# Kernel tuning notes

Measured on AMD Instinct MI355X. Metric: run time of the kernel, lower is better.

The kernel has to match this reference:

```python
import jax, jax.numpy as jnp
import numpy as np

B, S, D = 32, 2048, 1024


def setup_inputs() -> dict:
    key = jax.random.key(0)
    k = jax.random.split(key, 7)
    midi_features = jax.random.normal(k[0], (B, S, D), dtype=jnp.float32)
    scale_id = jax.random.randint(k[1], (B,), 0, 3)
    midi_mask = jax.random.randint(k[2], (B, S), 0, 2).astype(jnp.int32)
    # Stacked branch params: index 0=high, 1=mid, 2=low (matches SCALE_TO_ID)
    W = jax.random.normal(k[3], (3, D, D), dtype=jnp.float32) * 0.02  # Linear weight (out,in)
    b = jax.random.normal(k[4], (3, D), dtype=jnp.float32) * 0.02
    scale_embed = jax.random.normal(k[5], (3, D), dtype=jnp.float32) * 0.02
    branch_embed = jax.random.normal(k[6], (3, D), dtype=jnp.float32) * 0.02
    return {"midi_features": midi_features, "scale_id": scale_id, "midi_mask": midi_mask,
            "W": W, "b": b, "scale_embed": scale_embed, "branch_embed": branch_embed}


def reference(midi_features, scale_id, midi_mask, W, b, scale_embed, branch_embed):
    # Per-sample scale routing: gather the branch's Linear weight for each sample
    # (equivalent to the torch fancy-indexing scatter into out[idx]).
    Wb = W[scale_id]               # (B, D, D) torch Linear convention: y = x @ W.T + b
    bb = b[scale_id]               # (B, D)
    out = jax.nn.silu(jnp.einsum('bsd,bed->bse', midi_features, Wb) + bb[:, None, :])
    # Dropout is identity in eval mode.
    out = out + scale_embed[scale_id][:, None, :]       # (B, S, D)

    seq_mask = midi_mask > 0                             # (B, S) bool
    w = seq_mask.astype(out.dtype)[:, :, None]           # (B, S, 1)
    denom = jnp.maximum(w.sum(axis=1), 1e-6)             # (B, 1)
    low_vec = (out * w).sum(axis=1) / denom              # (B, D) masked mean

    high_cond = out + branch_embed[0]                    # (B, S, D)
    mid_cond = out + branch_embed[1]                     # (B, S, D)
    low_cond = low_vec[:, None, :] + branch_embed[2]     # (B, 1, D) weak_low_alignment=True
    return high_cond, mid_cond, low_cond
```

## Files before the change

### kernel.cpp

```cpp
#include <hip/hip_runtime.h>
#include <hip/hip_bf16.h>

#define B_ 32
#define S_ 2048
#define D_ 1024

#define BM 256
#define BN 128
#define BK 32
#define NKT (D_ / BK)

typedef __attribute__((ext_vector_type(8))) short bf16x8;
typedef __attribute__((ext_vector_type(4))) float f32x4;
typedef __attribute__((ext_vector_type(4))) float float4v;

#define AS1 __attribute__((address_space(1)))
#define AS3 __attribute__((address_space(3)))

__device__ __forceinline__ short f2bf(float f) {
    union { float f; unsigned u; } uf;
    uf.f = f;
    unsigned u = uf.u;
    u += 0x7FFFu + ((u >> 16) & 1u);
    return (short)(u >> 16);
}

__global__ __launch_bounds__(256) void cvt_bf16(const float4v* __restrict__ src,
                                                bf16x8* __restrict__ dst, int n8) {
    const int stride = gridDim.x * blockDim.x;
    for (int i = blockIdx.x * blockDim.x + threadIdx.x; i < n8; i += stride) {
        float4v a = src[2 * i], b = src[2 * i + 1];
        bf16x8 v;
#pragma unroll
        for (int j = 0; j < 4; ++j) {
            v[j]     = f2bf(a[j]);
            v[4 + j] = f2bf(b[j]);
        }
        dst[i] = v;
    }
}


#define STAGE(SB, kt) do {                                                     \
    const __hip_bfloat16* _ga0 = aBase + (size_t)srow * D_ + (kt) * BK + scol; \
    __builtin_amdgcn_global_load_lds((const AS1 unsigned int*)_ga0,            \
        (AS3 unsigned int*)((char*)&As[SB][0] + tid * 16), 16, 0, 0);          \
    const __hip_bfloat16* _ga1 = aBase + (size_t)(srow + 128) * D_ + (kt) * BK + scol; \
    __builtin_amdgcn_global_load_lds((const AS1 unsigned int*)_ga1,            \
        (AS3 unsigned int*)((char*)&As[SB][0] + 8192 + tid * 16), 16, 0, 0);   \
    const __hip_bfloat16* _gb = bBase + (size_t)srow * D_ + (kt) * BK + scol;  \
    __builtin_amdgcn_global_load_lds((const AS1 unsigned int*)_gb,             \
        (AS3 unsigned int*)((char*)&Bs[SB][0] + tid * 16), 16, 0, 0);          \
} while (0)

#define COMPUTE(CB) do {                                                       \
    bf16x8 _af[4], _bv[4];                                                     \
    _Pragma("unroll")                                                          \
    for (int _mi = 0; _mi < 4; ++_mi)                                          \
        _af[_mi] = *(const bf16x8*)((const char*)&As[CB][0] + aRd + _mi * 1024); \
    _Pragma("unroll")                                                          \
    for (int _ni = 0; _ni < 4; ++_ni)                                          \
        _bv[_ni] = *(const bf16x8*)((const char*)&Bs[CB][0] + bRd + _ni * 1024); \
    __builtin_amdgcn_s_setprio(1);                                             \
    _Pragma("unroll")                                                          \
    for (int _mi = 0; _mi < 4; ++_mi)                                          \
        _Pragma("unroll")                                                      \
        for (int _ni = 0; _ni < 4; ++_ni)                                      \
            acc[_mi][_ni] = __builtin_amdgcn_mfma_f32_16x16x32_bf16(           \
                _af[_mi], _bv[_ni], acc[_mi][_ni], 0, 0, 0);                   \
    __builtin_amdgcn_s_setprio(0); } while (0)

#define VMW(n)  asm volatile("s_waitcnt vmcnt(" #n ")" ::: "memory")
#define SBAR()  asm volatile("s_barrier" ::: "memory")

#define KITER(CB, SB, ktn) do { VMW(3); SBAR(); STAGE(SB, ktn); COMPUTE(CB); } while (0)

__global__ __launch_bounds__(512, 4) void fused_gemm_bf16(
    const __hip_bfloat16* __restrict__ aBf,
    const __hip_bfloat16* __restrict__ wBf,
    const int*   __restrict__ scale_id,
    const int*   __restrict__ mask,
    const float* __restrict__ bias,
    const float* __restrict__ scemb,
    const float* __restrict__ bremb,
    float*       __restrict__ out,
    float*       __restrict__ colws)
{
    __shared__ __align__(16) short As[3][BM * BK];
    __shared__ __align__(16) short Bs[3][BN * BK];

    const int tid = threadIdx.x;
    const int lane = tid & 63;
    const int wid = tid >> 6;
    const int wm = wid >> 1, wn = wid & 1;

    const int NTI = D_ / BN;
    const int MTI = S_ / BM;
    const int NWG = B_ * MTI * NTI;
    const int CPX = NWG / 8;
    int lid = ((int)blockIdx.x % 8) * CPX + ((int)blockIdx.x / 8);
    int nt = lid % NTI;
    int mt = (lid / NTI) % MTI;
    int bb = lid / (NTI * MTI);

    const int sid = scale_id[bb];
    const __hip_bfloat16* aBase = aBf + ((size_t)bb * S_ + (size_t)mt * BM) * D_;
    const __hip_bfloat16* bBase = wBf + ((size_t)sid * D_ + (size_t)nt * BN) * D_;

    const int l5 = tid & 31;
    const int ir0 = ((l5 >> 2) ^ (l5 >> 4)) & 1;
    const int ir1 = (l5 >> 3) & 1;
    const int ir2 = (l5 >> 4) & 1;
    const int is1 = ((l5 >> 1) ^ (l5 >> 3)) & 1;
    const int is0 = (l5 ^ (l5 >> 2) ^ (l5 >> 4)) & 1;
    const int srow = (tid >> 5) * 8 + ir2 * 4 + ir1 * 2 + ir0;
    const int scol = (is1 * 2 + is0) * 8;

    const int fr = lane & 15;
    const int fg = lane >> 4;
    const int aRd = (((wm * 64 + fr) * 64) + fg * 16) ^ ((fr & 7) << 4);
    const int bRd = (((wn * 64 + fr) * 64) + fg * 16) ^ ((fr & 7) << 4);

    f32x4 acc[4][4];
#pragma unroll
    for (int mi = 0; mi < 4; ++mi)
#pragma unroll
        for (int ni = 0; ni < 4; ++ni)
            acc[mi][ni] = (f32x4){0.f, 0.f, 0.f, 0.f};

    STAGE(0, 0);
    STAGE(1, 1);

#pragma unroll 1
    for (int t = 0; t < NKT - 2; t += 3) {
        KITER(0, 2, t + 2);
        KITER(1, 0, t + 3);
        KITER(2, 1, t + 4);
    }
    VMW(3); SBAR(); COMPUTE(0);
    VMW(0); SBAR(); COMPUTE(1);

    __syncthreads();

    const int colb = nt * BN;
    float bv[4], sv[4];
#pragma unroll
    for (int ni = 0; ni < 4; ++ni) {
        const int n = colb + wn * 64 + ni * 16 + fr;
        bv[ni] = bias[sid * D_ + n];
        sv[ni] = scemb[sid * D_ + n];
    }

    float colsum[4] = {0.f, 0.f, 0.f, 0.f};
#pragma unroll
    for (int mi = 0; mi < 4; ++mi) {
        const int mrow0 = mt * BM + wm * 64 + mi * 16 + fg * 4;
        float mk[4];
#pragma unroll
        for (int r = 0; r < 4; ++r)
            mk[r] = (mask[(size_t)bb * S_ + mrow0 + r] > 0) ? 1.f : 0.f;
#pragma unroll
        for (int ni = 0; ni < 4; ++ni)
#pragma unroll
            for (int r = 0; r < 4; ++r) {
                const float v = acc[mi][ni][r] + bv[ni];
                const float o = v / (1.f + __expf(-v)) + sv[ni];
                acc[mi][ni][r] = o;
                colsum[ni] += mk[r] * o;
            }
    }

#pragma unroll
    for (int ni = 0; ni < 4; ++ni) {
        float s = colsum[ni];
        s += __shfl_xor(s, 16);
        s += __shfl_xor(s, 32);
        if (fg == 0) {
            const int n = colb + wn * 64 + ni * 16 + fr;
            atomicAdd(&colws[(size_t)bb * D_ + n], s);
        }
    }

    float* ldsF = (float*)&As[0][0];
    const int lr = tid >> 3;
    const int c8 = tid & 7;

    float4v b0q[4], b1q[4];
#pragma unroll
    for (int q = 0; q < 4; ++q) {
        const int gcol = colb + q * 32 + c8 * 4;
        b0q[q] = *(const float4v*)&bremb[0 * D_ + gcol];
        b1q[q] = *(const float4v*)&bremb[1 * D_ + gcol];
    }

    const size_t MIDOFF = (size_t)B_ * S_ * D_;

#pragma unroll
    for (int mi = 0; mi < 4; ++mi) {
#pragma unroll
        for (int ni = 0; ni < 4; ++ni)
#pragma unroll
            for (int r = 0; r < 4; ++r)
                ldsF[(wm * 16 + fg * 4 + r) * 132 + wn * 64 + ni * 16 + fr] =
                    acc[mi][ni][r];
        __syncthreads();

        const int grow = mt * BM + (lr >> 4) * 64 + mi * 16 + (lr & 15);
        const size_t rowbase = ((size_t)bb * S_ + grow) * D_ + colb;
#pragma unroll
        for (int q = 0; q < 4; ++q) {
            float4v v = *(const float4v*)&ldsF[lr * 132 + q * 32 + c8 * 4];
            __builtin_nontemporal_store(v + b0q[q], (float4v*)&out[rowbase + q * 32 + c8 * 4]);
            __builtin_nontemporal_store(v + b1q[q], (float4v*)&out[MIDOFF + rowbase + q * 32 + c8 * 4]);
        }
        __syncthreads();
    }
}

#define FBM 128
#define FBN 128
#define FBK 64
#define FNK (D_ / FBK)

__global__ __launch_bounds__(256, 2) void fused_gemm_f32(
    const float* __restrict__ midi,
    const int*   __restrict__ scale_id,
    const int*   __restrict__ mask,
    const float* __restrict__ W,
    const float* __restrict__ bias,
    const float* __restrict__ scemb,
    const float* __restrict__ bremb,
    float*       __restrict__ out,
    float*       __restrict__ ws)
{
    __shared__ __align__(16) short Asf[FBM * FBK];
    __shared__ __align__(16) short Bsf[FBM * FBK];

    const int tid = threadIdx.x;
    const int NTI = D_ / FBN;
    const int MTI = S_ / FBM;
    const int NWG = B_ * MTI * NTI;
    const int CPX = NWG / 8;
    int lid = ((int)blockIdx.x % 8) * CPX + ((int)blockIdx.x / 8);
    int nt = lid % NTI;
    int mt = (lid / NTI) % MTI;
    int bb = lid / (NTI * MTI);

    const int sid = scale_id[bb];
    const float* aBase = midi + ((size_t)bb * S_ + (size_t)mt * FBM) * D_;
    const float* bBase = W + ((size_t)sid * D_ + (size_t)nt * FBN) * D_;

    const int r0 = tid >> 3;
    const int kp = (tid & 7) * 8;

    float4v aL[4], aH[4], bL[4], bH[4];

    auto load_regs = [&](int kt) {
        const int kc = kt * FBK + kp;
#pragma unroll
        for (int i = 0; i < 4; ++i) {
            const float* pa = aBase + (size_t)(r0 + 32 * i) * D_ + kc;
            aL[i] = *(const float4v*)pa;
            aH[i] = *(const float4v*)(pa + 4);
            const float* pb = bBase + (size_t)(r0 + 32 * i) * D_ + kc;
            bL[i] = *(const float4v*)pb;
            bH[i] = *(const float4v*)(pb + 4);
        }
    };

    auto write_lds = [&]() {
#pragma unroll
        for (int i = 0; i < 4; ++i) {
            const int row = r0 + 32 * i;
            const int off = (row * FBK + kp) ^ ((row & 7) << 3);
            bf16x8 va, vb;
#pragma unroll
            for (int j = 0; j < 4; ++j) {
                va[j]     = f2bf(aL[i][j]);
                va[4 + j] = f2bf(aH[i][j]);
                vb[j]     = f2bf(bL[i][j]);
                vb[4 + j] = f2bf(bH[i][j]);
            }
            *(bf16x8*)&Asf[off] = va;
            *(bf16x8*)&Bsf[off] = vb;
        }
    };

    f32x4 acc[4][4];
#pragma unroll
    for (int mi = 0; mi < 4; ++mi)
#pragma unroll
        for (int ni = 0; ni < 4; ++ni)
            acc[mi][ni] = (f32x4){0.f, 0.f, 0.f, 0.f};

    const int lane = tid & 63;
    const int wid = tid >> 6;
    const int wm = wid >> 1, wn = wid & 1;
    const int fr = lane & 15;
    const int fg = lane >> 4;

    load_regs(0);
    write_lds();
    __syncthreads();

    for (int kt = 0; kt < FNK; ++kt) {
        if (kt + 1 < FNK) load_regs(kt + 1);
#pragma unroll
        for (int kk = 0; kk < 2; ++kk) {
            bf16x8 af[4], bfr[4];
#pragma unroll
            for (int mi = 0; mi < 4; ++mi) {
                const int row = wm * 64 + mi * 16 + fr;
                const int off = (row * FBK + kk * 32 + fg * 8) ^ ((row & 7) << 3);
                af[mi] = *(const bf16x8*)&Asf[off];
            }
#pragma unroll
            for (int ni = 0; ni < 4; ++ni) {
                const int row = wn * 64 + ni * 16 + fr;
                const int off = (row * FBK + kk * 32 + fg * 8) ^ ((row & 7) << 3);
                bfr[ni] = *(const bf16x8*)&Bsf[off];
            }
#pragma unroll
            for (int mi = 0; mi < 4; ++mi)
#pragma unroll
                for (int ni = 0; ni < 4; ++ni)
                    acc[mi][ni] = __builtin_amdgcn_mfma_f32_16x16x32_bf16(
                        af[mi], bfr[ni], acc[mi][ni], 0, 0, 0);
        }
        __syncthreads();
        if (kt + 1 < FNK) write_lds();
        __syncthreads();
    }

    const int ncolbase = nt * FBN + wn * 64;
    float bv[4], sv[4], b0v[4], b1v[4];
#pragma unroll
    for (int ni = 0; ni < 4; ++ni) {
        const int n = ncolbase + ni * 16 + fr;
        bv[ni]  = bias[sid * D_ + n];
        sv[ni]  = scemb[sid * D_ + n];
        b0v[ni] = bremb[0 * D_ + n];
        b1v[ni] = bremb[1 * D_ + n];
    }

    const size_t MIDOFF = (size_t)B_ * S_ * D_;
    float colsum[4] = {0.f, 0.f, 0.f, 0.f};

#pragma unroll
    for (int mi = 0; mi < 4; ++mi) {
        const int mrow0 = mt * FBM + wm * 64 + mi * 16 + fg * 4;
        float mk[4];
#pragma unroll
        for (int r = 0; r < 4; ++r)
            mk[r] = (mask[(size_t)bb * S_ + mrow0 + r] > 0) ? 1.f : 0.f;
#pragma unroll
        for (int ni = 0; ni < 4; ++ni) {
            const int n = ncolbase + ni * 16 + fr;
#pragma unroll
            for (int r = 0; r < 4; ++r) {
                const float v = acc[mi][ni][r] + bv[ni];
                const float o = v / (1.f + __expf(-v)) + sv[ni];
                const size_t idx = ((size_t)bb * S_ + (size_t)(mrow0 + r)) * D_ + n;
                __builtin_nontemporal_store(o + b0v[ni], &out[idx]);
                __builtin_nontemporal_store(o + b1v[ni], &out[MIDOFF + idx]);
                colsum[ni] += mk[r] * o;
            }
        }
    }

#pragma unroll
    for (int ni = 0; ni < 4; ++ni) {
        float s = colsum[ni];
        s += __shfl_xor(s, 16);
        s += __shfl_xor(s, 32);
        if (fg == 0)
            atomicAdd(&ws[(size_t)bb * D_ + (ncolbase + ni * 16 + fr)], s);
    }
}

__global__ void finalize(const int* __restrict__ mask,
                         const float* __restrict__ ws,
                         const float* __restrict__ bremb,
                         float* __restrict__ out)
{
    const int b = blockIdx.x;
    const int tid = threadIdx.x;

    int c = 0;
    for (int s = tid; s < S_; s += 256)
        c += (mask[(size_t)b * S_ + s] > 0) ? 1 : 0;
#pragma unroll
    for (int m = 1; m < 64; m <<= 1)
        c += __shfl_xor(c, m);

    __shared__ int part[4];
    if ((tid & 63) == 0) part[tid >> 6] = c;
    __syncthreads();
    const float denom = fmaxf((float)(part[0] + part[1] + part[2] + part[3]), 1e-6f);
    const float inv = 1.f / denom;

    const size_t LOWOFF = (size_t)2 * B_ * S_ * D_;
    for (int e = tid; e < D_; e += 256)
        out[LOWOFF + (size_t)b * D_ + e] = ws[(size_t)b * D_ + e] * inv + bremb[2 * D_ + e];
}

extern "C" void kernel_launch(void* const* d_in, const int* in_sizes, int n_in,
                              void* d_out, int out_size, void* d_ws, size_t ws_size,
                              hipStream_t stream) {
    const float* midi     = (const float*)d_in[0];
    const int*   scale_id = (const int*)d_in[1];
    const int*   mask     = (const int*)d_in[2];
    const float* W        = (const float*)d_in[3];
    const float* bias     = (const float*)d_in[4];
    const float* scemb    = (const float*)d_in[5];
    const float* bremb    = (const float*)d_in[6];
    float* out = (float*)d_out;
    float* colws = (float*)d_ws;

    const size_t COLWS_B = (size_t)B_ * D_ * sizeof(float);
    const size_t WBF_B   = (size_t)3 * D_ * D_ * sizeof(short);
    const size_t ABF_B   = (size_t)B_ * S_ * D_ * sizeof(short);
    const size_t need    = COLWS_B + WBF_B + ABF_B;

    hipMemsetAsync(colws, 0, COLWS_B, stream);

    if (ws_size >= need) {
        __hip_bfloat16* wBf = (__hip_bfloat16*)((char*)d_ws + COLWS_B);
        __hip_bfloat16* aBf = (__hip_bfloat16*)((char*)d_ws + COLWS_B + WBF_B);
        cvt_bf16<<<dim3(2048), dim3(256), 0, stream>>>(
            (const float4v*)midi, (bf16x8*)aBf, (B_ * S_ * D_) / 8);
        cvt_bf16<<<dim3(512), dim3(256), 0, stream>>>(
            (const float4v*)W, (bf16x8*)wBf, (3 * D_ * D_) / 8);
        fused_gemm_bf16<<<dim3(B_ * (S_ / BM) * (D_ / BN)), dim3(512), 0, stream>>>(
            aBf, wBf, scale_id, mask, bias, scemb, bremb, out, colws);
    } else {
        fused_gemm_f32<<<dim3(B_ * (S_ / FBM) * (D_ / FBN)), dim3(256), 0, stream>>>(
            midi, scale_id, mask, W, bias, scemb, bremb, out, colws);
    }

    finalize<<<dim3(B_), dim3(256), 0, stream>>>(mask, colws, bremb, out);
}
```

Measured before the change: 345.5 us.

## Retile bf16 GEMM to 256x64x64 with 4 waves and split-phase double buffering

Changes the bf16 GEMM tile from 256x128 with BK=32 and 8 waves to 256x64 with BK=64 and 4 waves. Each wave now computes two 64-row halves, and the A/B stage loads are split across two half-iterations so loads overlap with compute on a two-buffer LDS ring. The LDS swizzle and the epilogue store layout are redone to match the new tile. Narrower N tiles double the grid size and re-read A twice as often, traded for lower LDS footprint and finer-grained load/compute interleaving.

```diff
diff --git a/kernel.cpp b/kernel.cpp
--- a/kernel.cpp
+++ b/kernel.cpp
@@ -6,8 +6,8 @@
 #define D_ 1024
 
 #define BM 256
-#define BN 128
-#define BK 32
+#define BN 64
+#define BK 64
 #define NKT (D_ / BK)
 
 typedef __attribute__((ext_vector_type(8))) short bf16x8;
@@ -41,41 +41,69 @@
 }
 
 
-#define STAGE(SB, kt) do {                                                     \
-    const __hip_bfloat16* _ga0 = aBase + (size_t)srow * D_ + (kt) * BK + scol; \
-    __builtin_amdgcn_global_load_lds((const AS1 unsigned int*)_ga0,            \
-        (AS3 unsigned int*)((char*)&As[SB][0] + tid * 16), 16, 0, 0);          \
-    const __hip_bfloat16* _ga1 = aBase + (size_t)(srow + 128) * D_ + (kt) * BK + scol; \
-    __builtin_amdgcn_global_load_lds((const AS1 unsigned int*)_ga1,            \
-        (AS3 unsigned int*)((char*)&As[SB][0] + 8192 + tid * 16), 16, 0, 0);   \
-    const __hip_bfloat16* _gb = bBase + (size_t)srow * D_ + (kt) * BK + scol;  \
-    __builtin_amdgcn_global_load_lds((const AS1 unsigned int*)_gb,             \
-        (AS3 unsigned int*)((char*)&Bs[SB][0] + tid * 16), 16, 0, 0);          \
-} while (0)
-
-#define COMPUTE(CB) do {                                                       \
-    bf16x8 _af[4], _bv[4];                                                     \
+#define STAGE_A(nb, p, kt) do {                                                \
     _Pragma("unroll")                                                          \
-    for (int _mi = 0; _mi < 4; ++_mi)                                          \
-        _af[_mi] = *(const bf16x8*)((const char*)&As[CB][0] + aRd + _mi * 1024); \
+    for (int _j = 0; _j < 4; ++_j) {                                           \
+        const int _r = (_j >> 1) * 128 + (p) * 64 + (_j & 1) * 32 + wid * 8 + lrow8; \
+        const __hip_bfloat16* _g = aBase + (size_t)_r * D_ + (kt) * BK + (scb >> 1); \
+        __builtin_amdgcn_global_load_lds((const AS1 unsigned int*)_g,          \
+            (AS3 unsigned int*)&As[nb][_r * 64 + (lane & 7) * 8], 16, 0, 0);   \
+    } } while (0)
+
+#define STAGE_B(nb, kt) do {                                                   \
     _Pragma("unroll")                                                          \
-    for (int _ni = 0; _ni < 4; ++_ni)                                          \
-        _bv[_ni] = *(const bf16x8*)((const char*)&Bs[CB][0] + bRd + _ni * 1024); \
+    for (int _j = 0; _j < 2; ++_j) {                                           \
+        const int _r = _j * 32 + wid * 8 + lrow8;                              \
+        const __hip_bfloat16* _g = bBase + (size_t)_r * D_ + (kt) * BK + (scb >> 1); \
+        __builtin_amdgcn_global_load_lds((const AS1 unsigned int*)_g,          \
+            (AS3 unsigned int*)&Bs[nb][_r * 64 + (lane & 7) * 8], 16, 0, 0);   \
+    } } while (0)
+
+#define COMPUTE(cur, p) do {                                                   \
+    bf16x8 _af[4][2], _bv[2][2];                                               \
+    _Pragma("unroll")                                                          \
+    for (int _mi = 0; _mi < 4; ++_mi) {                                        \
+        const int _l = wm * 128 + (p) * 64 + _mi * 16 + fr;                    \
+        _Pragma("unroll")                                                      \
+        for (int _kk = 0; _kk < 2; ++_kk) {                                    \
+            const int _b = _l * 128 + ((_kk * 64 + fg * 16) ^ ((_l & 7) << 4)); \
+            _af[_mi][_kk] = *(const bf16x8*)((const char*)&As[cur][0] + _b);   \
+        }                                                                      \
+    }                                                                          \
+    _Pragma("unroll")                                                          \
+    for (int _ni = 0; _ni < 2; ++_ni) {                                        \
+        const int _l = wn * 32 + _ni * 16 + fr;                                \
+        _Pragma("unroll")                                                      \
+        for (int _kk = 0; _kk < 2; ++_kk) {                                    \
+            const int _b = _l * 128 + ((_kk * 64 + fg * 16) ^ ((_l & 7) << 4)); \
+            _bv[_ni][_kk] = *(const bf16x8*)((const char*)&Bs[cur][0] + _b);   \
+        }                                                                      \
+    }                                                                          \
     __builtin_amdgcn_s_setprio(1);                                             \
     _Pragma("unroll")                                                          \
     for (int _mi = 0; _mi < 4; ++_mi)                                          \
         _Pragma("unroll")                                                      \
-        for (int _ni = 0; _ni < 4; ++_ni)                                      \
-            acc[_mi][_ni] = __builtin_amdgcn_mfma_f32_16x16x32_bf16(           \
-                _af[_mi], _bv[_ni], acc[_mi][_ni], 0, 0, 0);                   \
+        for (int _ni = 0; _ni < 2; ++_ni)                                      \
+            _Pragma("unroll")                                                  \
+            for (int _kk = 0; _kk < 2; ++_kk)                                  \
+                acc[p][_mi][_ni] = __builtin_amdgcn_mfma_f32_16x16x32_bf16(    \
+                    _af[_mi][_kk], _bv[_ni][_kk], acc[p][_mi][_ni], 0, 0, 0);  \
     __builtin_amdgcn_s_setprio(0); } while (0)
 
 #define VMW(n)  asm volatile("s_waitcnt vmcnt(" #n ")" ::: "memory")
 #define SBAR()  asm volatile("s_barrier" ::: "memory")
 
-#define KITER(CB, SB, ktn) do { VMW(3); SBAR(); STAGE(SB, ktn); COMPUTE(CB); } while (0)
-
-__global__ __launch_bounds__(512, 4) void fused_gemm_bf16(
+#define KITER(X, Y, ktn) do {                                                  \
+    STAGE_A(Y, 0, ktn); VMW(8);  SBAR(); COMPUTE(X, 0);                        \
+    STAGE_B(Y, ktn); STAGE_A(Y, 1, ktn); VMW(10); SBAR(); COMPUTE(X, 1);       \
+} while (0)
+
+#define KTAIL(X) do {                                                          \
+    VMW(4); SBAR(); COMPUTE(X, 0);                                             \
+    VMW(0); SBAR(); COMPUTE(X, 1);                                             \
+} while (0)
+
+__global__ __launch_bounds__(256, 2) void fused_gemm_bf16(
     const __hip_bfloat16* __restrict__ aBf,
     const __hip_bfloat16* __restrict__ wBf,
     const int*   __restrict__ scale_id,
@@ -86,8 +114,8 @@
     float*       __restrict__ out,
     float*       __restrict__ colws)
 {
-    __shared__ __align__(16) short As[3][BM * BK];
-    __shared__ __align__(16) short Bs[3][BN * BK];
+    __shared__ __align__(16) short As[2][BM * BK];
+    __shared__ __align__(16) short Bs[2][BN * BK];
 
     const int tid = threadIdx.x;
     const int lane = tid & 63;
@@ -107,114 +135,105 @@
     const __hip_bfloat16* aBase = aBf + ((size_t)bb * S_ + (size_t)mt * BM) * D_;
     const __hip_bfloat16* bBase = wBf + ((size_t)sid * D_ + (size_t)nt * BN) * D_;
 
-    const int l5 = tid & 31;
-    const int ir0 = ((l5 >> 2) ^ (l5 >> 4)) & 1;
-    const int ir1 = (l5 >> 3) & 1;
-    const int ir2 = (l5 >> 4) & 1;
-    const int is1 = ((l5 >> 1) ^ (l5 >> 3)) & 1;
-    const int is0 = (l5 ^ (l5 >> 2) ^ (l5 >> 4)) & 1;
-    const int srow = (tid >> 5) * 8 + ir2 * 4 + ir1 * 2 + ir0;
-    const int scol = (is1 * 2 + is0) * 8;
+    const int lrow8 = lane >> 3;
+    const int scb = ((lane & 7) * 16) ^ (lrow8 << 4);
 
     const int fr = lane & 15;
     const int fg = lane >> 4;
-    const int aRd = (((wm * 64 + fr) * 64) + fg * 16) ^ ((fr & 7) << 4);
-    const int bRd = (((wn * 64 + fr) * 64) + fg * 16) ^ ((fr & 7) << 4);
-
-    f32x4 acc[4][4];
-#pragma unroll
-    for (int mi = 0; mi < 4; ++mi)
-#pragma unroll
-        for (int ni = 0; ni < 4; ++ni)
-            acc[mi][ni] = (f32x4){0.f, 0.f, 0.f, 0.f};
-
-    STAGE(0, 0);
-    STAGE(1, 1);
+
+    f32x4 acc[2][4][2];
+#pragma unroll
+    for (int p = 0; p < 2; ++p)
+#pragma unroll
+        for (int mi = 0; mi < 4; ++mi)
+#pragma unroll
+            for (int ni = 0; ni < 2; ++ni)
+                acc[p][mi][ni] = (f32x4){0.f, 0.f, 0.f, 0.f};
+
+    STAGE_A(0, 0, 0);
+    STAGE_B(0, 0);
+    STAGE_A(0, 1, 0);
 
 #pragma unroll 1
-    for (int t = 0; t < NKT - 2; t += 3) {
-        KITER(0, 2, t + 2);
-        KITER(1, 0, t + 3);
-        KITER(2, 1, t + 4);
-    }
-    VMW(3); SBAR(); COMPUTE(0);
-    VMW(0); SBAR(); COMPUTE(1);
-
+    for (int t = 0; t < NKT - 2; t += 2) {
+        KITER(0, 1, t + 1);
+        KITER(1, 0, t + 2);
+    }
+    KITER(0, 1, NKT - 1);
+    KTAIL(1);
+
+    asm volatile("s_waitcnt vmcnt(0) lgkmcnt(0)" ::: "memory");
     __syncthreads();
 
     const int colb = nt * BN;
-    float bv[4], sv[4];
-#pragma unroll
-    for (int ni = 0; ni < 4; ++ni) {
-        const int n = colb + wn * 64 + ni * 16 + fr;
+    float bv[2], sv[2];
+#pragma unroll
+    for (int ni = 0; ni < 2; ++ni) {
+        const int n = colb + wn * 32 + ni * 16 + fr;
         bv[ni] = bias[sid * D_ + n];
         sv[ni] = scemb[sid * D_ + n];
     }
 
-    float colsum[4] = {0.f, 0.f, 0.f, 0.f};
-#pragma unroll
-    for (int mi = 0; mi < 4; ++mi) {
-        const int mrow0 = mt * BM + wm * 64 + mi * 16 + fg * 4;
-        float mk[4];
-#pragma unroll
-        for (int r = 0; r < 4; ++r)
-            mk[r] = (mask[(size_t)bb * S_ + mrow0 + r] > 0) ? 1.f : 0.f;
-#pragma unroll
-        for (int ni = 0; ni < 4; ++ni)
-#pragma unroll
-            for (int r = 0; r < 4; ++r) {
-                const float v = acc[mi][ni][r] + bv[ni];
-                const float o = v / (1.f + __expf(-v)) + sv[ni];
-                acc[mi][ni][r] = o;
-                colsum[ni] += mk[r] * o;
-            }
-    }
-
-#pragma unroll
-    for (int ni = 0; ni < 4; ++ni) {
+    float colsum[2] = {0.f, 0.f};
+#pragma unroll
+    for (int p = 0; p < 2; ++p)
+#pragma unroll
+        for (int mi = 0; mi < 4; ++mi) {
+            const int mrow0 = mt * BM + wm * 128 + p * 64 + mi * 16 + fg * 4;
+            float mk[4];
+#pragma unroll
+            for (int r = 0; r < 4; ++r)
+                mk[r] = (mask[(size_t)bb * S_ + mrow0 + r] > 0) ? 1.f : 0.f;
+#pragma unroll
+            for (int ni = 0; ni < 2; ++ni)
+#pragma unroll
+                for (int r = 0; r < 4; ++r) {
+                    const float v = acc[p][mi][ni][r] + bv[ni];
+                    const float o = v / (1.f + __expf(-v)) + sv[ni];
+                    acc[p][mi][ni][r] = o;
+                    colsum[ni] += mk[r] * o;
+                }
+        }
+
+#pragma unroll
+    for (int ni = 0; ni < 2; ++ni) {
         float s = colsum[ni];
         s += __shfl_xor(s, 16);
         s += __shfl_xor(s, 32);
         if (fg == 0) {
-            const int n = colb + wn * 64 + ni * 16 + fr;
+            const int n = colb + wn * 32 + ni * 16 + fr;
             atomicAdd(&colws[(size_t)bb * D_ + n], s);
         }
     }
 
     float* ldsF = (float*)&As[0][0];
-    const int lr = tid >> 3;
-    const int c8 = tid & 7;
-
-    float4v b0q[4], b1q[4];
-#pragma unroll
-    for (int q = 0; q < 4; ++q) {
-        const int gcol = colb + q * 32 + c8 * 4;
-        b0q[q] = *(const float4v*)&bremb[0 * D_ + gcol];
-        b1q[q] = *(const float4v*)&bremb[1 * D_ + gcol];
-    }
-
+    const float4v b0 = *(const float4v*)&bremb[0 * D_ + colb + (tid & 15) * 4];
+    const float4v b1 = *(const float4v*)&bremb[1 * D_ + colb + (tid & 15) * 4];
     const size_t MIDOFF = (size_t)B_ * S_ * D_;
 
 #pragma unroll
-    for (int mi = 0; mi < 4; ++mi) {
-#pragma unroll
-        for (int ni = 0; ni < 4; ++ni)
-#pragma unroll
-            for (int r = 0; r < 4; ++r)
-                ldsF[(wm * 16 + fg * 4 + r) * 132 + wn * 64 + ni * 16 + fr] =
-                    acc[mi][ni][r];
-        __syncthreads();
-
-        const int grow = mt * BM + (lr >> 4) * 64 + mi * 16 + (lr & 15);
-        const size_t rowbase = ((size_t)bb * S_ + grow) * D_ + colb;
-#pragma unroll
-        for (int q = 0; q < 4; ++q) {
-            float4v v = *(const float4v*)&ldsF[lr * 132 + q * 32 + c8 * 4];
-            __builtin_nontemporal_store(v + b0q[q], (float4v*)&out[rowbase + q * 32 + c8 * 4]);
-            __builtin_nontemporal_store(v + b1q[q], (float4v*)&out[MIDOFF + rowbase + q * 32 + c8 * 4]);
-        }
-        __syncthreads();
-    }
+    for (int p = 0; p < 2; ++p)
+#pragma unroll
+        for (int mi = 0; mi < 4; ++mi) {
+#pragma unroll
+            for (int ni = 0; ni < 2; ++ni)
+#pragma unroll
+                for (int r = 0; r < 4; ++r)
+                    ldsF[(wm * 16 + fg * 4 + r) * 68 + wn * 32 + ni * 16 + fr] =
+                        acc[p][mi][ni][r];
+            __syncthreads();
+
+#pragma unroll
+            for (int k = 0; k < 2; ++k) {
+                const int lrow = k * 16 + (tid >> 4);
+                const int grow = mt * BM + (lrow >> 4) * 128 + p * 64 + mi * 16 + (lrow & 15);
+                const size_t rowbase = ((size_t)bb * S_ + grow) * D_ + colb;
+                float4v v = *(const float4v*)&ldsF[lrow * 68 + (tid & 15) * 4];
+                __builtin_nontemporal_store(v + b0, (float4v*)&out[rowbase + (tid & 15) * 4]);
+                __builtin_nontemporal_store(v + b1, (float4v*)&out[MIDOFF + rowbase + (tid & 15) * 4]);
+            }
+            __syncthreads();
+        }
 }
 
 #define FBM 128
@@ -431,7 +450,7 @@
             (const float4v*)midi, (bf16x8*)aBf, (B_ * S_ * D_) / 8);
         cvt_bf16<<<dim3(512), dim3(256), 0, stream>>>(
             (const float4v*)W, (bf16x8*)wBf, (3 * D_ * D_) / 8);
-        fused_gemm_bf16<<<dim3(B_ * (S_ / BM) * (D_ / BN)), dim3(512), 0, stream>>>(
+        fused_gemm_bf16<<<dim3(B_ * (S_ / BM) * (D_ / BN)), dim3(256), 0, stream>>>(
             aBf, wBf, scale_id, mask, bias, scemb, bremb, out, colws);
     } else {
         fused_gemm_f32<<<dim3(B_ * (S_ / FBM) * (D_ / FBN)), dim3(256), 0, stream>>>(
```

Measured after the change: 415.5 us. +20.3%, slower.

## Enlarge bf16 GEMM tile to 256x256 with split-phase LDS/MFMA pipeline

Applied to the files above, without the earlier changes.

Doubles the N tile to 256, so each wave computes a 128x64 sub-tile with eight M fragments. The K loop is restructured into two half-phases: the B and first-half A fragments are read from LDS and their MFMAs issued while the next A stage loads, then the second A half is read while the next B stage loads, with explicit barriers and lgkm waits. The epilogue is rewritten for the wider tile, with each wave storing full 256-column rows. The aim is more arithmetic per byte loaded and better overlap of loads with MFMA, at the cost of more registers, occupancy lowered to 2 blocks, and more barriers.

```diff
diff --git a/kernel.cpp b/kernel.cpp
--- a/kernel.cpp
+++ b/kernel.cpp
@@ -6,7 +6,7 @@
 #define D_ 1024
 
 #define BM 256
-#define BN 128
+#define BN 256
 #define BK 32
 #define NKT (D_ / BK)
 
@@ -41,41 +41,101 @@
 }
 
 
-#define STAGE(SB, kt) do {                                                     \
-    const __hip_bfloat16* _ga0 = aBase + (size_t)srow * D_ + (kt) * BK + scol; \
-    __builtin_amdgcn_global_load_lds((const AS1 unsigned int*)_ga0,            \
-        (AS3 unsigned int*)((char*)&As[SB][0] + tid * 16), 16, 0, 0);          \
-    const __hip_bfloat16* _ga1 = aBase + (size_t)(srow + 128) * D_ + (kt) * BK + scol; \
-    __builtin_amdgcn_global_load_lds((const AS1 unsigned int*)_ga1,            \
-        (AS3 unsigned int*)((char*)&As[SB][0] + 8192 + tid * 16), 16, 0, 0);   \
-    const __hip_bfloat16* _gb = bBase + (size_t)srow * D_ + (kt) * BK + scol;  \
-    __builtin_amdgcn_global_load_lds((const AS1 unsigned int*)_gb,             \
-        (AS3 unsigned int*)((char*)&Bs[SB][0] + tid * 16), 16, 0, 0);          \
+#define STAGE_A(S, kt) do {                                                    \
+    const __hip_bfloat16* _g0 = aBase + (size_t)srow * D_ + (kt) * BK + scol;  \
+    __builtin_amdgcn_global_load_lds((const AS1 unsigned int*)_g0,             \
+        (AS3 unsigned int*)((char*)&As[S][0] + tid * 16), 16, 0, 0);           \
+    const __hip_bfloat16* _g1 = aBase + (size_t)(srow + 128) * D_ + (kt) * BK + scol; \
+    __builtin_amdgcn_global_load_lds((const AS1 unsigned int*)_g1,             \
+        (AS3 unsigned int*)((char*)&As[S][0] + 8192 + tid * 16), 16, 0, 0);    \
 } while (0)
 
-#define COMPUTE(CB) do {                                                       \
-    bf16x8 _af[4], _bv[4];                                                     \
+#define STAGE_B(S, kt) do {                                                    \
+    const __hip_bfloat16* _g0 = bBase + (size_t)srow * D_ + (kt) * BK + scol;  \
+    __builtin_amdgcn_global_load_lds((const AS1 unsigned int*)_g0,             \
+        (AS3 unsigned int*)((char*)&Bs[S][0] + tid * 16), 16, 0, 0);           \
+    const __hip_bfloat16* _g1 = bBase + (size_t)(srow + 128) * D_ + (kt) * BK + scol; \
+    __builtin_amdgcn_global_load_lds((const AS1 unsigned int*)_g1,             \
+        (AS3 unsigned int*)((char*)&Bs[S][0] + 8192 + tid * 16), 16, 0, 0);    \
+} while (0)
+
+#define DSLOAD_B(C) do {                                                       \
     _Pragma("unroll")                                                          \
-    for (int _mi = 0; _mi < 4; ++_mi)                                          \
-        _af[_mi] = *(const bf16x8*)((const char*)&As[CB][0] + aRd + _mi * 1024); \
+    for (int _n = 0; _n < 4; ++_n) {                                           \
+        const int _l = wn * 64 + _n * 16 + fr;                                 \
+        fB[_n] = *(const bf16x8*)((const char*)&Bs[C][0] +                     \
+                  ((_l * 64 + fg * 16) ^ ((_l & 7) << 4)));                    \
+    } } while (0)
+
+#define DSLOAD_A0(C) do {                                                      \
     _Pragma("unroll")                                                          \
-    for (int _ni = 0; _ni < 4; ++_ni)                                          \
-        _bv[_ni] = *(const bf16x8*)((const char*)&Bs[CB][0] + bRd + _ni * 1024); \
+    for (int _m = 0; _m < 4; ++_m) {                                           \
+        const int _l = wm * 128 + _m * 16 + fr;                                \
+        fA0[_m] = *(const bf16x8*)((const char*)&As[C][0] +                    \
+                  ((_l * 64 + fg * 16) ^ ((_l & 7) << 4)));                    \
+    } } while (0)
+
+#define DSLOAD_A1(C) do {                                                      \
+    _Pragma("unroll")                                                          \
+    for (int _m = 0; _m < 4; ++_m) {                                           \
+        const int _l = wm * 128 + 64 + _m * 16 + fr;                           \
+        fA1[_m] = *(const bf16x8*)((const char*)&As[C][0] +                    \
+                  ((_l * 64 + fg * 16) ^ ((_l & 7) << 4)));                    \
+    } } while (0)
+
+#define MMA_H0() do {                                                          \
     __builtin_amdgcn_s_setprio(1);                                             \
     _Pragma("unroll")                                                          \
-    for (int _mi = 0; _mi < 4; ++_mi)                                          \
+    for (int _m = 0; _m < 4; ++_m)                                             \
         _Pragma("unroll")                                                      \
-        for (int _ni = 0; _ni < 4; ++_ni)                                      \
-            acc[_mi][_ni] = __builtin_amdgcn_mfma_f32_16x16x32_bf16(           \
-                _af[_mi], _bv[_ni], acc[_mi][_ni], 0, 0, 0);                   \
+        for (int _n = 0; _n < 4; ++_n)                                         \
+            acc[_m][_n] = __builtin_amdgcn_mfma_f32_16x16x32_bf16(             \
+                fA0[_m], fB[_n], acc[_m][_n], 0, 0, 0);                        \
     __builtin_amdgcn_s_setprio(0); } while (0)
 
+#define MMA_H1() do {                                                          \
+    __builtin_amdgcn_s_setprio(1);                                             \
+    _Pragma("unroll")                                                          \
+    for (int _m = 0; _m < 4; ++_m)                                             \
+        _Pragma("unroll")                                                      \
+        for (int _n = 0; _n < 4; ++_n)                                         \
+            acc[4 + _m][_n] = __builtin_amdgcn_mfma_f32_16x16x32_bf16(         \
+                fA1[_m], fB[_n], acc[4 + _m][_n], 0, 0, 0);                    \
+    __builtin_amdgcn_s_setprio(0); } while (0)
+
 #define VMW(n)  asm volatile("s_waitcnt vmcnt(" #n ")" ::: "memory")
+#define LGKM0() asm volatile("s_waitcnt lgkmcnt(0)" ::: "memory")
+#define SCHB()  __builtin_amdgcn_sched_barrier(0)
 #define SBAR()  asm volatile("s_barrier" ::: "memory")
 
-#define KITER(CB, SB, ktn) do { VMW(3); SBAR(); STAGE(SB, ktn); COMPUTE(CB); } while (0)
-
-__global__ __launch_bounds__(512, 4) void fused_gemm_bf16(
+#define TILE(C, S, kn) do {                                                    \
+    DSLOAD_B(C); DSLOAD_A0(C);                                                 \
+    STAGE_A(S, kn);                                                            \
+    SBAR(); LGKM0(); SCHB();                                                   \
+    MMA_H0();                                                                  \
+    SBAR();                                                                    \
+    DSLOAD_A1(C);                                                              \
+    STAGE_B(S, kn);                                                            \
+    VMW(4); SBAR(); LGKM0(); SCHB();                                           \
+    MMA_H1();                                                                  \
+    SBAR();                                                                    \
+} while (0)
+
+#define TILE_T30(C) do {                                                       \
+    DSLOAD_B(C); DSLOAD_A0(C);                                                 \
+    SBAR(); LGKM0(); SCHB(); MMA_H0(); SBAR();                                 \
+    DSLOAD_A1(C);                                                              \
+    VMW(0); SBAR(); LGKM0(); SCHB(); MMA_H1(); SBAR();                         \
+} while (0)
+
+#define TILE_T31(C) do {                                                       \
+    DSLOAD_B(C); DSLOAD_A0(C);                                                 \
+    SBAR(); LGKM0(); SCHB(); MMA_H0(); SBAR();                                 \
+    DSLOAD_A1(C);                                                              \
+    SBAR(); LGKM0(); SCHB(); MMA_H1(); SBAR();                                 \
+} while (0)
+
+__global__ __launch_bounds__(512, 2) void fused_gemm_bf16(
     const __hip_bfloat16* __restrict__ aBf,
     const __hip_bfloat16* __restrict__ wBf,
     const int*   __restrict__ scale_id,
@@ -92,7 +152,8 @@
     const int tid = threadIdx.x;
     const int lane = tid & 63;
     const int wid = tid >> 6;
-    const int wm = wid >> 1, wn = wid & 1;
+    const int wm = wid >> 2;
+    const int wn = wid & 3;
 
     const int NTI = D_ / BN;
     const int MTI = S_ / BM;
@@ -118,27 +179,28 @@
 
     const int fr = lane & 15;
     const int fg = lane >> 4;
-    const int aRd = (((wm * 64 + fr) * 64) + fg * 16) ^ ((fr & 7) << 4);
-    const int bRd = (((wn * 64 + fr) * 64) + fg * 16) ^ ((fr & 7) << 4);
-
-    f32x4 acc[4][4];
-#pragma unroll
-    for (int mi = 0; mi < 4; ++mi)
+
+    f32x4 acc[8][4];
+#pragma unroll
+    for (int mi = 0; mi < 8; ++mi)
 #pragma unroll
         for (int ni = 0; ni < 4; ++ni)
             acc[mi][ni] = (f32x4){0.f, 0.f, 0.f, 0.f};
 
-    STAGE(0, 0);
-    STAGE(1, 1);
+    bf16x8 fA0[4], fA1[4], fB[4];
+
+    STAGE_A(0, 0); STAGE_B(0, 0);
+    STAGE_A(1, 1); STAGE_B(1, 1);
+    VMW(4); SBAR();
 
 #pragma unroll 1
     for (int t = 0; t < NKT - 2; t += 3) {
-        KITER(0, 2, t + 2);
-        KITER(1, 0, t + 3);
-        KITER(2, 1, t + 4);
-    }
-    VMW(3); SBAR(); COMPUTE(0);
-    VMW(0); SBAR(); COMPUTE(1);
+        TILE(0, 2, t + 2);
+        TILE(1, 0, t + 3);
+        TILE(2, 1, t + 4);
+    }
+    TILE_T30(0);
+    TILE_T31(1);
 
     __syncthreads();
 
@@ -153,8 +215,8 @@
 
     float colsum[4] = {0.f, 0.f, 0.f, 0.f};
 #pragma unroll
-    for (int mi = 0; mi < 4; ++mi) {
-        const int mrow0 = mt * BM + wm * 64 + mi * 16 + fg * 4;
+    for (int mi = 0; mi < 8; ++mi) {
+        const int mrow0 = mt * BM + wm * 128 + mi * 16 + fg * 4;
         float mk[4];
 #pragma unroll
         for (int r = 0; r < 4; ++r)
@@ -182,36 +244,28 @@
     }
 
     float* ldsF = (float*)&As[0][0];
-    const int lr = tid >> 3;
-    const int c8 = tid & 7;
-
-    float4v b0q[4], b1q[4];
-#pragma unroll
-    for (int q = 0; q < 4; ++q) {
-        const int gcol = colb + q * 32 + c8 * 4;
-        b0q[q] = *(const float4v*)&bremb[0 * D_ + gcol];
-        b1q[q] = *(const float4v*)&bremb[1 * D_ + gcol];
-    }
-
+    const float4v b0 = *(const float4v*)&bremb[0 * D_ + colb + lane * 4];
+    const float4v b1 = *(const float4v*)&bremb[1 * D_ + colb + lane * 4];
     const size_t MIDOFF = (size_t)B_ * S_ * D_;
 
 #pragma unroll
-    for (int mi = 0; mi < 4; ++mi) {
+    for (int mi = 0; mi < 8; ++mi) {
 #pragma unroll
         for (int ni = 0; ni < 4; ++ni)
 #pragma unroll
             for (int r = 0; r < 4; ++r)
-                ldsF[(wm * 16 + fg * 4 + r) * 132 + wn * 64 + ni * 16 + fr] =
+                ldsF[(wm * 16 + fg * 4 + r) * 260 + wn * 64 + ni * 16 + fr] =
                     acc[mi][ni][r];
         __syncthreads();
 
-        const int grow = mt * BM + (lr >> 4) * 64 + mi * 16 + (lr & 15);
-        const size_t rowbase = ((size_t)bb * S_ + grow) * D_ + colb;
-#pragma unroll
-        for (int q = 0; q < 4; ++q) {
-            float4v v = *(const float4v*)&ldsF[lr * 132 + q * 32 + c8 * 4];
-            __builtin_nontemporal_store(v + b0q[q], (float4v*)&out[rowbase + q * 32 + c8 * 4]);
-            __builtin_nontemporal_store(v + b1q[q], (float4v*)&out[MIDOFF + rowbase + q * 32 + c8 * 4]);
+#pragma unroll
+        for (int k = 0; k < 4; ++k) {
+            const int lr = wid * 4 + k;
+            const int grow = mt * BM + (lr >> 4) * 128 + mi * 16 + (lr & 15);
+            const size_t rowbase = ((size_t)bb * S_ + grow) * D_ + colb;
+            float4v v = *(const float4v*)&ldsF[lr * 260 + lane * 4];
+            __builtin_nontemporal_store(v + b0, (float4v*)&out[rowbase + lane * 4]);
+            __builtin_nontemporal_store(v + b1, (float4v*)&out[MIDOFF + rowbase + lane * 4]);
         }
         __syncthreads();
     }
```

Result: faster. 312.6 us (-9.5%).
